# Performance work log

Hardware: AMD Instinct MI355X
Metric: run time of the kernel (lower is better)

The kernel has to match this reference:

```python
import jax, jax.numpy as jnp
import numpy as np

CLS_NUM, INPUT_DIM, BATCH = 1024, 512, 16384
TAU = 0.1       # gumbel-softmax temperature from F.gumbel_softmax(sim, tau=0.1)
EPS = 1e-12     # F.normalize eps


def _l2norm(x):
    # F.normalize(x, p=2, dim=1)
    n = jnp.sqrt(jnp.sum(x * x, axis=1, keepdims=True))
    return x / jnp.maximum(n, EPS)


def setup_inputs() -> dict:
    key = jax.random.key(0)
    k1, k2, k3 = jax.random.split(key, 3)
    # xavier_uniform bound for [cls_num, input_dim]
    bound = float(np.sqrt(6.0 / (CLS_NUM + INPUT_DIM)))
    return {
        "input": jax.random.normal(k1, (BATCH, INPUT_DIM), dtype=jnp.float32),
        "prototypes_para": jax.random.uniform(k2, (CLS_NUM, INPUT_DIM), dtype=jnp.float32, minval=-bound, maxval=bound),
        "gumbel_u": jax.random.uniform(k3, (BATCH, CLS_NUM), dtype=jnp.float32, minval=1e-6, maxval=1.0 - 1e-6),
    }


def reference(input, prototypes_para, gumbel_u):
    x = _l2norm(input)                 # [B, D]
    p = _l2norm(prototypes_para)       # [K, D]
    # Original: broadcast x and p to [B, K, D] (via multiply-by-ones) then cosine.
    # Since both are unit-norm, cosine similarity == dot product -> one matmul.
    # Input is .detach()'d in the original, so stop_gradient on x here.
    sim = jax.lax.stop_gradient(x) @ p.T                    # [B, K]
    # Gumbel-softmax (soft): softmax((logits + gumbel)/tau)
    g = -jnp.log(-jnp.log(gumbel_u))
    e = jax.nn.softmax((sim + g) / TAU, axis=-1)            # [B, K]
    pt = jnp.einsum('bk,kv->bv', e, p)                      # [B, D]
    sim_loss = jnp.mean(1.0 - jnp.einsum('bk,bk->b', e, sim))
    # Nested i!=j pairwise cosine loop == sum of P P^T minus its diagonal
    ppt = p @ p.T                                           # [K, K]
    div_loss = jnp.sum(ppt) - jnp.sum(jnp.diagonal(ppt))
    return pt, p, sim_loss, div_loss
```

## Files before the change

kernel.cpp:

```cpp
#include <hip/hip_runtime.h>
#include <math.h>

#define B  16384
#define K  1024
#define D  512
#define TAU_INV 10.0f
#define EPS 1e-12f

typedef unsigned short ushort_t;

#define OUT_PT   0
#define OUT_P    (B*D)
#define OUT_SIM  (B*D + K*D)
#define OUT_DIV  (B*D + K*D + 1)

#define WS_RED   1024
#define WS_SIM   32768
#define WS_PH    (WS_SIM + (B*K)/2)
#define WS_PTH   (WS_PH + (K*D)/2)
#define WS_DIAGP (WS_PTH + (K*D)/2)
#define WS_COLP  (WS_DIAGP + 256)


typedef _Float16 half8 __attribute__((ext_vector_type(8)));
typedef float f32x4 __attribute__((ext_vector_type(4)));

__device__ __forceinline__ float wave_reduce_sum(float v) {
    #pragma unroll
    for (int off = 32; off >= 1; off >>= 1) v += __shfl_down(v, off);
    return v;
}
__device__ __forceinline__ float wave_reduce_max(float v) {
    #pragma unroll
    for (int off = 32; off >= 1; off >>= 1) v = fmaxf(v, __shfl_down(v, off));
    return v;
}

__device__ __forceinline__ ushort_t f2h(float f) {
    _Float16 h = (_Float16)f;
    return __builtin_bit_cast(ushort_t, h);
}
__device__ __forceinline__ float h2f(ushort_t u) {
    return (float)__builtin_bit_cast(_Float16, u);
}

__device__ __forceinline__ void async16(const void* g, void* l) {
    __builtin_amdgcn_global_load_lds(
        (const __attribute__((address_space(1))) unsigned int*)g,
        (__attribute__((address_space(3))) unsigned int*)l, 16, 0, 0);
}

__global__ __launch_bounds__(256) void norm_p_kernel(const float* __restrict__ proto,
                                                     float* __restrict__ out,
                                                     float* __restrict__ ws,
                                                     ushort_t* __restrict__ Ph) {
    __shared__ float cs[4][512];
    __shared__ float red[4];
    int tid = threadIdx.x, wid = tid >> 6, lane = tid & 63;
    int row = blockIdx.x * 4 + wid;
    const float4* pr = (const float4*)(proto + (size_t)row * D);
    float4 a = pr[lane * 2], b = pr[lane * 2 + 1];
    float ss = a.x*a.x + a.y*a.y + a.z*a.z + a.w*a.w
             + b.x*b.x + b.y*b.y + b.z*b.z + b.w*b.w;
    ss = wave_reduce_sum(ss);
    ss = __shfl(ss, 0);
    float inv = 1.0f / fmaxf(sqrtf(ss), EPS);
    float4 na = make_float4(a.x*inv, a.y*inv, a.z*inv, a.w*inv);
    float4 nb = make_float4(b.x*inv, b.y*inv, b.z*inv, b.w*inv);
    float4* po = (float4*)(out + OUT_P + (size_t)row * D);
    po[lane * 2]     = na;
    po[lane * 2 + 1] = nb;
    ushort4* ph = (ushort4*)(Ph + (size_t)row * D);
    ph[lane * 2]     = make_ushort4(f2h(na.x), f2h(na.y), f2h(na.z), f2h(na.w));
    ph[lane * 2 + 1] = make_ushort4(f2h(nb.x), f2h(nb.y), f2h(nb.z), f2h(nb.w));
    *(float4*)(&cs[wid][lane * 8])     = na;
    *(float4*)(&cs[wid][lane * 8 + 4]) = nb;
    if (lane == 0) red[wid] = ss * inv * inv;
    __syncthreads();
    float c0 = cs[0][tid] + cs[1][tid] + cs[2][tid] + cs[3][tid];
    float c1 = cs[0][tid + 256] + cs[1][tid + 256] + cs[2][tid + 256] + cs[3][tid + 256];
    ws[WS_COLP + (size_t)blockIdx.x * 512 + tid]       = c0;
    ws[WS_COLP + (size_t)blockIdx.x * 512 + tid + 256] = c1;
    if (tid == 0) ws[WS_DIAGP + blockIdx.x] = red[0] + red[1] + red[2] + red[3];
}

__global__ __launch_bounds__(256) void ptcvt_kernel(const float* __restrict__ out,
                                                    ushort_t* __restrict__ PT) {
    __shared__ float tile[64][65];
    int k0 = blockIdx.x * 64, d0 = blockIdx.y * 64;
    int tid = threadIdx.x;
    const float* phat = out + OUT_P;
    #pragma unroll
    for (int i = tid; i < 64 * 64; i += 256) {
        int kk = i >> 6, dd = i & 63;
        tile[dd][kk] = phat[(size_t)(k0 + kk) * D + d0 + dd];
    }
    __syncthreads();
    #pragma unroll
    for (int i = tid; i < 64 * 64; i += 256) {
        int dd = i >> 6, kk = i & 63;
        PT[(size_t)(d0 + dd) * K + k0 + kk] = f2h(tile[dd][kk]);
    }
}

__global__ __launch_bounds__(256) void xcvt_kernel(const float* __restrict__ x,
                                                   ushort_t* __restrict__ Xh) {
    int wid = threadIdx.x >> 6, lane = threadIdx.x & 63;
    int row = blockIdx.x * 4 + wid;
    const float4* xr = (const float4*)(x + (size_t)row * D);
    float4 a = xr[lane * 2], b = xr[lane * 2 + 1];
    float ss = a.x*a.x + a.y*a.y + a.z*a.z + a.w*a.w
             + b.x*b.x + b.y*b.y + b.z*b.z + b.w*b.w;
    ss = wave_reduce_sum(ss);
    ss = __shfl(ss, 0);
    float inv = 1.0f / fmaxf(sqrtf(ss), EPS);
    ushort4 h0 = make_ushort4(f2h(a.x*inv), f2h(a.y*inv), f2h(a.z*inv), f2h(a.w*inv));
    ushort4 h1 = make_ushort4(f2h(b.x*inv), f2h(b.y*inv), f2h(b.z*inv), f2h(b.w*inv));
    ushort4* xo = (ushort4*)(Xh + (size_t)row * D);
    xo[lane * 2]     = h0;
    xo[lane * 2 + 1] = h1;
}

template<int LDA, int LDB, int LDC, int KK, bool F16C>
__global__ __launch_bounds__(256) void gemm_bt2(const ushort_t* __restrict__ A,
                                                const ushort_t* __restrict__ Bm,
                                                void* __restrict__ Cv) {
    __shared__ __align__(16) ushort_t As[2 * 128 * 32];
    __shared__ __align__(16) ushort_t Bs[2 * 128 * 32];
    int tid = threadIdx.x;
    int wid = tid >> 6, lane = tid & 63;
    int quad = lane >> 4, l16 = lane & 15;
    int wm = (wid & 1) * 64, wn = (wid >> 1) * 64;
    int bn0 = blockIdx.x * 128, bm0 = blockIdx.y * 128;
    int ldrow = lane >> 2;
    int lcol  = (lane & 3) * 8;

    f32x4 acc[4][4] = {};

    ushort_t* AsD[2][2] = {
        { As + (wid * 16) * 32,        As + (64 + wid * 16) * 32 },
        { As + 4096 + (wid * 16) * 32, As + 4096 + (64 + wid * 16) * 32 } };
    ushort_t* BsD[2][2] = {
        { Bs + (wid * 16) * 32,        Bs + (64 + wid * 16) * 32 },
        { Bs + 4096 + (wid * 16) * 32, Bs + 4096 + (64 + wid * 16) * 32 } };

    const ushort_t* Ab = A + (size_t)(bm0 + wid * 16 + ldrow) * LDA + lcol;
    const ushort_t* Bb = Bm + (size_t)(bn0 + wid * 16 + ldrow) * LDB + lcol;

    for (int kc = 0; kc < KK; kc += 64) {
        async16(Ab + kc,                       AsD[0][0]);
        async16(Ab + kc + (size_t)64 * LDA,    AsD[0][1]);
        async16(Ab + kc + 32,                  AsD[1][0]);
        async16(Ab + kc + 32 + (size_t)64*LDA, AsD[1][1]);
        async16(Bb + kc,                       BsD[0][0]);
        async16(Bb + kc + (size_t)64 * LDB,    BsD[0][1]);
        async16(Bb + kc + 32,                  BsD[1][0]);
        async16(Bb + kc + 32 + (size_t)64*LDB, BsD[1][1]);
        __syncthreads();
        #pragma unroll
        for (int p = 0; p < 2; ++p) {
            half8 af[4], bg[4];
            #pragma unroll
            for (int i = 0; i < 4; ++i)
                af[i] = *(const half8*)(As + p * 4096 + (wm + 16 * i + l16) * 32 + quad * 8);
            #pragma unroll
            for (int j = 0; j < 4; ++j)
                bg[j] = *(const half8*)(Bs + p * 4096 + (wn + 16 * j + l16) * 32 + quad * 8);
            #pragma unroll
            for (int i = 0; i < 4; ++i)
                #pragma unroll
                for (int j = 0; j < 4; ++j)
                    acc[i][j] = __builtin_amdgcn_mfma_f32_16x16x32_f16(af[i], bg[j], acc[i][j], 0, 0, 0);
        }
        __syncthreads();
    }
    #pragma unroll
    for (int i = 0; i < 4; ++i) {
        #pragma unroll
        for (int j = 0; j < 4; ++j) {
            #pragma unroll
            for (int r = 0; r < 4; ++r) {
                int row = bm0 + wm + 16 * i + quad * 4 + r;
                int col = bn0 + wn + 16 * j + l16;
                if (F16C)
                    ((ushort_t*)Cv)[(size_t)row * LDC + col] = f2h(acc[i][j][r]);
                else
                    ((float*)Cv)[(size_t)row * LDC + col] = acc[i][j][r];
            }
        }
    }
}

__global__ __launch_bounds__(256) void softmax_rows(const float* __restrict__ u,
                                                    float* __restrict__ ws) {
    ushort_t* simh = (ushort_t*)(ws + WS_SIM);
    int tid = threadIdx.x;
    int wid = tid >> 6, lane = tid & 63;
    int gw = blockIdx.x * 4 + wid;
    float dotacc = 0.0f;

    for (int r = 0; r < 4; ++r) {
        int row = gw + 4096 * r;
        ushort4* srow = (ushort4*)(simh + (size_t)row * K);
        const float4* urow = (const float4*)(u + (size_t)row * K);
        float4 s[4], z[4];
        #pragma unroll
        for (int j = 0; j < 4; ++j) {
            ushort4 sh = srow[lane + 64 * j];
            float4 uu = urow[lane + 64 * j];
            s[j] = make_float4(h2f(sh.x), h2f(sh.y), h2f(sh.z), h2f(sh.w));
            z[j].x = (s[j].x - logf(-logf(uu.x))) * TAU_INV;
            z[j].y = (s[j].y - logf(-logf(uu.y))) * TAU_INV;
            z[j].z = (s[j].z - logf(-logf(uu.z))) * TAU_INV;
            z[j].w = (s[j].w - logf(-logf(uu.w))) * TAU_INV;
        }
        float m = z[0].x;
        #pragma unroll
        for (int j = 0; j < 4; ++j)
            m = fmaxf(m, fmaxf(fmaxf(z[j].x, z[j].y), fmaxf(z[j].z, z[j].w)));
        m = wave_reduce_max(m);
        m = __shfl(m, 0);

        float4 e[4];
        float l = 0.0f;
        #pragma unroll
        for (int j = 0; j < 4; ++j) {
            e[j].x = expf(z[j].x - m);
            e[j].y = expf(z[j].y - m);
            e[j].z = expf(z[j].z - m);
            e[j].w = expf(z[j].w - m);
            l += e[j].x + e[j].y + e[j].z + e[j].w;
        }
        l = wave_reduce_sum(l);
        l = __shfl(l, 0);
        float inv = 1.0f / l;

        #pragma unroll
        for (int j = 0; j < 4; ++j) {
            float ex = e[j].x * inv, ey = e[j].y * inv,
                  ez = e[j].z * inv, ew = e[j].w * inv;
            srow[lane + 64 * j] = make_ushort4(f2h(ex), f2h(ey), f2h(ez), f2h(ew));
            dotacc += ex * s[j].x + ey * s[j].y + ez * s[j].z + ew * s[j].w;
        }
    }

    dotacc = wave_reduce_sum(dotacc);
    __shared__ float red[4];
    if (lane == 0) red[wid] = dotacc;
    __syncthreads();
    if (tid == 0) ws[WS_RED + blockIdx.x] = red[0] + red[1] + red[2] + red[3];
}

__global__ __launch_bounds__(256) void finalize_kernel(float* __restrict__ out,
                                                       const float* __restrict__ ws) {
    int tid = threadIdx.x, wid = tid >> 6, lane = tid & 63;
    float vdot = 0.0f;
    #pragma unroll
    for (int i = 0; i < 4; ++i) vdot += ws[WS_RED + tid + 256 * i];
    float diag = ws[WS_DIAGP + tid];
    float c0 = 0.0f, c1 = 0.0f;
    for (int b2 = 0; b2 < 256; ++b2) {
        c0 += ws[WS_COLP + (size_t)b2 * 512 + tid];
        c1 += ws[WS_COLP + (size_t)b2 * 512 + tid + 256];
    }
    float vssq = c0 * c0 + c1 * c1;
    vdot = wave_reduce_sum(vdot);
    vssq = wave_reduce_sum(vssq);
    diag = wave_reduce_sum(diag);
    __shared__ float rd[4], rs[4], rg[4];
    if (lane == 0) { rd[wid] = vdot; rs[wid] = vssq; rg[wid] = diag; }
    __syncthreads();
    if (tid == 0) {
        float dot = rd[0] + rd[1] + rd[2] + rd[3];
        float ssq = rs[0] + rs[1] + rs[2] + rs[3];
        float dg  = rg[0] + rg[1] + rg[2] + rg[3];
        out[OUT_SIM] = 1.0f - dot * (1.0f / (float)B);
        out[OUT_DIV] = ssq - dg;
    }
}

extern "C" void kernel_launch(void* const* d_in, const int* in_sizes, int n_in,
                              void* d_out, int out_size, void* d_ws, size_t ws_size,
                              hipStream_t stream) {
    const float* input  = (const float*)d_in[0];
    const float* proto  = (const float*)d_in[1];
    const float* gumbel = (const float*)d_in[2];
    float* out = (float*)d_out;
    float* ws  = (float*)d_ws;

    ushort_t* Xh   = (ushort_t*)(out + OUT_PT);
    ushort_t* Ph   = (ushort_t*)(ws + WS_PH);
    ushort_t* PTh  = (ushort_t*)(ws + WS_PTH);
    ushort_t* simh = (ushort_t*)(ws + WS_SIM);

    norm_p_kernel<<<K / 4, 256, 0, stream>>>(proto, out, ws, Ph);
    {
        dim3 grid(K / 64, D / 64);
        ptcvt_kernel<<<grid, 256, 0, stream>>>(out, PTh);
    }
    xcvt_kernel<<<B / 4, 256, 0, stream>>>(input, Xh);
    {
        dim3 grid(K / 128, B / 128);
        gemm_bt2<512, 512, K, 512, true><<<grid, 256, 0, stream>>>(Xh, Ph, simh);
    }
    softmax_rows<<<1024, 256, 0, stream>>>(gumbel, ws);
    {
        dim3 grid(D / 128, B / 128);
        gemm_bt2<1024, 1024, D, 1024, false><<<grid, 256, 0, stream>>>(simh, PTh, out + OUT_PT);
    }
    finalize_kernel<<<1, 256, 0, stream>>>(out, ws);
}
```

Before: 221.3 us.

## Fuse similarity GEMM with gumbel-softmax into one full-row kernel

Replaces the separate X·Pᵀ GEMM and row softmax kernels with one kernel. Each 1024-thread block computes a 32×1024 strip of similarities held in registers and runs the gumbel-softmax and the loss dot product in place, using log2/exp2 intrinsics with folded constants. Only the fp16 softmax output is written back, so the fp16 sim round trip through global memory goes away. In exchange the whole P tile (128 KB LDS) is reloaded for every block, and with only 512 large blocks occupancy is low, with little overlap between loads and MFMA.

Measured after the change: 242.2 us. 1.09x slower.

```diff
diff --git a/kernel.cpp b/kernel.cpp
--- a/kernel.cpp
+++ b/kernel.cpp
@@ -4,10 +4,15 @@
 #define B  16384
 #define K  1024
 #define D  512
-#define TAU_INV 10.0f
 #define EPS 1e-12f
 
+#define SM_C1 14.426950408889634f
+#define SM_C2 5.287663729448977f
+
 typedef unsigned short ushort_t;
+
+#define LOG2F(x) __builtin_amdgcn_logf(x)
+#define EXP2F(x) __builtin_amdgcn_exp2f(x)
 
 #define OUT_PT   0
 #define OUT_P    (B*D)
@@ -28,11 +33,6 @@
 __device__ __forceinline__ float wave_reduce_sum(float v) {
     #pragma unroll
     for (int off = 32; off >= 1; off >>= 1) v += __shfl_down(v, off);
-    return v;
-}
-__device__ __forceinline__ float wave_reduce_max(float v) {
-    #pragma unroll
-    for (int off = 32; off >= 1; off >>= 1) v = fmaxf(v, __shfl_down(v, off));
     return v;
 }
 
@@ -121,6 +121,176 @@
     xo[lane * 2 + 1] = h1;
 }
 
+__global__ __launch_bounds__(1024) void simsm_kernel(const ushort_t* __restrict__ Xh,
+                                                     const ushort_t* __restrict__ Ph,
+                                                     const float* __restrict__ gum,
+                                                     ushort_t* __restrict__ Eh,
+                                                     float* __restrict__ ws) {
+    __shared__ __align__(16) ushort_t Bs[K * 64];
+    __shared__ __align__(16) ushort_t As[32 * 64];
+    __shared__ float wredM[16][32];
+    __shared__ float wredS[16][32];
+    __shared__ float wredD[16][32];
+    __shared__ float rowM[32];
+    __shared__ float rowInv[32];
+    __shared__ float rowDotA[32];
+
+    int tid = threadIdx.x;
+    int wid = tid >> 6, lane = tid & 63;
+    int quad = lane >> 4, l16 = lane & 15;
+    int wn = wid * 64;
+    int bm0 = blockIdx.x * 32;
+
+    f32x4 acc[2][4] = {};
+
+    float gu[2][4][4];
+    #pragma unroll
+    for (int i = 0; i < 2; ++i)
+        #pragma unroll
+        for (int j = 0; j < 4; ++j)
+            #pragma unroll
+            for (int r = 0; r < 4; ++r)
+                gu[i][j][r] = gum[(size_t)(bm0 + 16*i + 4*quad + r) * K + wn + 16*j + l16];
+
+    int csub = tid & 7;
+    for (int kc = 0; kc < 512; kc += 64) {
+        #pragma unroll
+        for (int r = 0; r < 8; ++r) {
+            int c = r * 1024 + tid;
+            int row = c >> 3;
+            async16(Ph + (size_t)row * 512 + kc + (((c & 7) ^ (row & 7)) << 3),
+                    Bs + ((size_t)r * 1024 + wid * 64) * 8);
+        }
+        if (wid < 4) {
+            int row = tid >> 3;
+            async16(Xh + (size_t)(bm0 + row) * 512 + kc + ((csub ^ (row & 7)) << 3),
+                    As + (size_t)(wid * 64) * 8);
+        }
+        __syncthreads();
+        half8 af[2][2];
+        #pragma unroll
+        for (int i = 0; i < 2; ++i)
+            #pragma unroll
+            for (int p = 0; p < 2; ++p) {
+                int rowl = 16*i + l16;
+                int chunk = (p*4 + quad) ^ (rowl & 7);
+                af[i][p] = *(const half8*)(As + rowl * 64 + chunk * 8);
+            }
+        #pragma unroll
+        for (int j = 0; j < 4; ++j) {
+            int rowl = wn + 16*j + l16;
+            int ch0 = quad ^ (rowl & 7);
+            int ch1 = (4 + quad) ^ (rowl & 7);
+            half8 b0 = *(const half8*)(Bs + rowl * 64 + ch0 * 8);
+            half8 b1 = *(const half8*)(Bs + rowl * 64 + ch1 * 8);
+            #pragma unroll
+            for (int i = 0; i < 2; ++i) {
+                acc[i][j] = __builtin_amdgcn_mfma_f32_16x16x32_f16(af[i][0], b0, acc[i][j], 0, 0, 0);
+                acc[i][j] = __builtin_amdgcn_mfma_f32_16x16x32_f16(af[i][1], b1, acc[i][j], 0, 0, 0);
+            }
+        }
+        __syncthreads();
+    }
+
+    float zz[2][4][4];
+    #pragma unroll
+    for (int i = 0; i < 2; ++i)
+        #pragma unroll
+        for (int j = 0; j < 4; ++j)
+            #pragma unroll
+            for (int r = 0; r < 4; ++r) {
+                float t = -LOG2F(gu[i][j][r]);
+                float l2t = LOG2F(t);
+                zz[i][j][r] = SM_C1 * acc[i][j][r] - 10.0f * l2t + SM_C2;
+            }
+
+    float mx[2][4];
+    #pragma unroll
+    for (int i = 0; i < 2; ++i)
+        #pragma unroll
+        for (int r = 0; r < 4; ++r) {
+            float m = fmaxf(fmaxf(zz[i][0][r], zz[i][1][r]),
+                            fmaxf(zz[i][2][r], zz[i][3][r]));
+            m = fmaxf(m, __shfl_xor(m, 1));
+            m = fmaxf(m, __shfl_xor(m, 2));
+            m = fmaxf(m, __shfl_xor(m, 4));
+            m = fmaxf(m, __shfl_xor(m, 8));
+            mx[i][r] = m;
+        }
+    if (l16 == 0) {
+        #pragma unroll
+        for (int i = 0; i < 2; ++i)
+            #pragma unroll
+            for (int r = 0; r < 4; ++r)
+                wredM[wid][16*i + 4*quad + r] = mx[i][r];
+    }
+    __syncthreads();
+    if (tid < 32) {
+        float m = wredM[0][tid];
+        #pragma unroll
+        for (int w = 1; w < 16; ++w) m = fmaxf(m, wredM[w][tid]);
+        rowM[tid] = m;
+    }
+    __syncthreads();
+
+    #pragma unroll
+    for (int i = 0; i < 2; ++i)
+        #pragma unroll
+        for (int r = 0; r < 4; ++r) {
+            float m = rowM[16*i + 4*quad + r];
+            float eacc = 0.0f, dacc = 0.0f;
+            #pragma unroll
+            for (int j = 0; j < 4; ++j) {
+                float e = EXP2F(zz[i][j][r] - m);
+                zz[i][j][r] = e;
+                eacc += e;
+                dacc += e * acc[i][j][r];
+            }
+            eacc += __shfl_xor(eacc, 1); dacc += __shfl_xor(dacc, 1);
+            eacc += __shfl_xor(eacc, 2); dacc += __shfl_xor(dacc, 2);
+            eacc += __shfl_xor(eacc, 4); dacc += __shfl_xor(dacc, 4);
+            eacc += __shfl_xor(eacc, 8); dacc += __shfl_xor(dacc, 8);
+            if (l16 == 0) {
+                wredS[wid][16*i + 4*quad + r] = eacc;
+                wredD[wid][16*i + 4*quad + r] = dacc;
+            }
+        }
+    __syncthreads();
+    if (tid < 32) {
+        float s = 0.0f, dd = 0.0f;
+        #pragma unroll
+        for (int w = 0; w < 16; ++w) { s += wredS[w][tid]; dd += wredD[w][tid]; }
+        rowInv[tid] = 1.0f / s;
+        rowDotA[tid] = dd / s;
+    }
+    __syncthreads();
+
+    ushort_t* Et = Bs;
+    #pragma unroll
+    for (int i = 0; i < 2; ++i)
+        #pragma unroll
+        for (int r = 0; r < 4; ++r) {
+            int row = 16*i + 4*quad + r;
+            float inv = rowInv[row];
+            #pragma unroll
+            for (int j = 0; j < 4; ++j)
+                Et[row * K + wn + 16*j + l16] = f2h(zz[i][j][r] * inv);
+        }
+    if (tid == 0) {
+        float dsum = 0.0f;
+        #pragma unroll
+        for (int k = 0; k < 32; ++k) dsum += rowDotA[k];
+        ws[WS_RED + blockIdx.x] = dsum;
+    }
+    __syncthreads();
+    {
+        int row = tid >> 5, seg = tid & 31;
+        const uint4* src = (const uint4*)(Et + row * K + seg * 32);
+        uint4* dst = (uint4*)(Eh + (size_t)(bm0 + row) * K + seg * 32);
+        dst[0] = src[0]; dst[1] = src[1]; dst[2] = src[2]; dst[3] = src[3];
+    }
+}
+
 template<int LDA, int LDB, int LDC, int KK, bool F16C>
 __global__ __launch_bounds__(256) void gemm_bt2(const ushort_t* __restrict__ A,
                                                 const ushort_t* __restrict__ Bm,
@@ -191,72 +361,10 @@
     }
 }
 
-__global__ __launch_bounds__(256) void softmax_rows(const float* __restrict__ u,
-                                                    float* __restrict__ ws) {
-    ushort_t* simh = (ushort_t*)(ws + WS_SIM);
-    int tid = threadIdx.x;
-    int wid = tid >> 6, lane = tid & 63;
-    int gw = blockIdx.x * 4 + wid;
-    float dotacc = 0.0f;
-
-    for (int r = 0; r < 4; ++r) {
-        int row = gw + 4096 * r;
-        ushort4* srow = (ushort4*)(simh + (size_t)row * K);
-        const float4* urow = (const float4*)(u + (size_t)row * K);
-        float4 s[4], z[4];
-        #pragma unroll
-        for (int j = 0; j < 4; ++j) {
-            ushort4 sh = srow[lane + 64 * j];
-            float4 uu = urow[lane + 64 * j];
-            s[j] = make_float4(h2f(sh.x), h2f(sh.y), h2f(sh.z), h2f(sh.w));
-            z[j].x = (s[j].x - logf(-logf(uu.x))) * TAU_INV;
-            z[j].y = (s[j].y - logf(-logf(uu.y))) * TAU_INV;
-            z[j].z = (s[j].z - logf(-logf(uu.z))) * TAU_INV;
-            z[j].w = (s[j].w - logf(-logf(uu.w))) * TAU_INV;
-        }
-        float m = z[0].x;
-        #pragma unroll
-        for (int j = 0; j < 4; ++j)
-            m = fmaxf(m, fmaxf(fmaxf(z[j].x, z[j].y), fmaxf(z[j].z, z[j].w)));
-        m = wave_reduce_max(m);
-        m = __shfl(m, 0);
-
-        float4 e[4];
-        float l = 0.0f;
-        #pragma unroll
-        for (int j = 0; j < 4; ++j) {
-            e[j].x = expf(z[j].x - m);
-            e[j].y = expf(z[j].y - m);
-            e[j].z = expf(z[j].z - m);
-            e[j].w = expf(z[j].w - m);
-            l += e[j].x + e[j].y + e[j].z + e[j].w;
-        }
-        l = wave_reduce_sum(l);
-        l = __shfl(l, 0);
-        float inv = 1.0f / l;
-
-        #pragma unroll
-        for (int j = 0; j < 4; ++j) {
-            float ex = e[j].x * inv, ey = e[j].y * inv,
-                  ez = e[j].z * inv, ew = e[j].w * inv;
-            srow[lane + 64 * j] = make_ushort4(f2h(ex), f2h(ey), f2h(ez), f2h(ew));
-            dotacc += ex * s[j].x + ey * s[j].y + ez * s[j].z + ew * s[j].w;
-        }
-    }
-
-    dotacc = wave_reduce_sum(dotacc);
-    __shared__ float red[4];
-    if (lane == 0) red[wid] = dotacc;
-    __syncthreads();
-    if (tid == 0) ws[WS_RED + blockIdx.x] = red[0] + red[1] + red[2] + red[3];
-}
-
 __global__ __launch_bounds__(256) void finalize_kernel(float* __restrict__ out,
                                                        const float* __restrict__ ws) {
     int tid = threadIdx.x, wid = tid >> 6, lane = tid & 63;
-    float vdot = 0.0f;
-    #pragma unroll
-    for (int i = 0; i < 4; ++i) vdot += ws[WS_RED + tid + 256 * i];
+    float vdot = ws[WS_RED + tid] + ws[WS_RED + tid + 256];
     float diag = ws[WS_DIAGP + tid];
     float c0 = 0.0f, c1 = 0.0f;
     for (int b2 = 0; b2 < 256; ++b2) {
@@ -291,7 +399,7 @@
     ushort_t* Xh   = (ushort_t*)(out + OUT_PT);
     ushort_t* Ph   = (ushort_t*)(ws + WS_PH);
     ushort_t* PTh  = (ushort_t*)(ws + WS_PTH);
-    ushort_t* simh = (ushort_t*)(ws + WS_SIM);
+    ushort_t* Eh   = (ushort_t*)(ws + WS_SIM);
 
     norm_p_kernel<<<K / 4, 256, 0, stream>>>(proto, out, ws, Ph);
     {
@@ -299,14 +407,10 @@
         ptcvt_kernel<<<grid, 256, 0, stream>>>(out, PTh);
     }
     xcvt_kernel<<<B / 4, 256, 0, stream>>>(input, Xh);
-    {
-        dim3 grid(K / 128, B / 128);
-        gemm_bt2<512, 512, K, 512, true><<<grid, 256, 0, stream>>>(Xh, Ph, simh);
-    }
-    softmax_rows<<<1024, 256, 0, stream>>>(gumbel, ws);
+    simsm_kernel<<<B / 32, 1024, 0, stream>>>(Xh, Ph, gumbel, Eh, ws);
     {
         dim3 grid(D / 128, B / 128);
-        gemm_bt2<1024, 1024, D, 1024, false><<<grid, 256, 0, stream>>>(simh, PTh, out + OUT_PT);
+        gemm_bt2<1024, 1024, D, 1024, false><<<grid, 256, 0, stream>>>(Eh, PTh, out + OUT_PT);
     }
     finalize_kernel<<<1, 256, 0, stream>>>(out, ws);
 }
```
